# Kernel optimization log

Hardware: AMD Instinct MI355X
Metric: run time of the kernel (lower is better)

The kernel has to match this reference:

```python
import jax, jax.numpy as jnp
import numpy as np

MIN_ROUGHNESS = 0.08
MAX_ROUGHNESS = 0.5
N_MIPS = 6  # 512 -> 16 cubemap mip chain


def _safe_normalize(x, eps=1e-20):
    return x * jax.lax.rsqrt(jnp.clip(jnp.sum(x * x, -1, keepdims=True), eps, None))


def _dot(a, b):
    return jnp.sum(a * b, -1, keepdims=True)


def _cube_face_uv(d):
    # nvdiffrast cube addressing (matches util.cube_to_dir face layout)
    x, y, z = d[..., 0], d[..., 1], d[..., 2]
    ax, ay, az = jnp.abs(x), jnp.abs(y), jnp.abs(z)
    is_x = (ax >= ay) & (ax >= az)
    is_y = (~is_x) & (ay >= az)
    face = jnp.where(is_x, jnp.where(x >= 0, 0, 1),
           jnp.where(is_y, jnp.where(y >= 0, 2, 3), jnp.where(z >= 0, 4, 5)))
    ma = jnp.maximum(jnp.where(is_x, ax, jnp.where(is_y, ay, az)), 1e-20)
    u = jnp.where(face == 0, -z, jnp.where(face == 1, z, jnp.where(face == 5, -x, x))) / ma
    v = jnp.where(face == 2, z, jnp.where(face == 3, -z, -y)) / ma
    return face, u, v


def _bilinear_cube(tex, face, u, v):
    # tex: [6,R,R,C]; face/u/v: [...]; edge-clamped bilinear within the face
    R = tex.shape[1]
    tu = (u * 0.5 + 0.5) * R - 0.5
    tv = (v * 0.5 + 0.5) * R - 0.5
    x0 = jnp.floor(tu); y0 = jnp.floor(tv)
    fx = (tu - x0)[..., None]; fy = (tv - y0)[..., None]
    x0i = jnp.clip(x0, 0, R - 1).astype(jnp.int32)
    x1i = jnp.clip(x0 + 1, 0, R - 1).astype(jnp.int32)
    y0i = jnp.clip(y0, 0, R - 1).astype(jnp.int32)
    y1i = jnp.clip(y0 + 1, 0, R - 1).astype(jnp.int32)
    c00 = tex[face, y0i, x0i]; c01 = tex[face, y0i, x1i]
    c10 = tex[face, y1i, x0i]; c11 = tex[face, y1i, x1i]
    return (c00 * (1 - fx) + c01 * fx) * (1 - fy) + (c10 * (1 - fx) + c11 * fx) * fy


def _sample_cubemap(tex, dirs):
    f, u, v = _cube_face_uv(dirs)
    return _bilinear_cube(tex, f, u, v)


def _sample_2d_clamp(tex, uv):
    # tex: [H,W,C]; uv in [0,1]^2, clamp boundary bilinear (FG LUT lookup)
    H, W = tex.shape[0], tex.shape[1]
    tu = uv[..., 0] * W - 0.5
    tv = uv[..., 1] * H - 0.5
    x0 = jnp.floor(tu); y0 = jnp.floor(tv)
    fx = (tu - x0)[..., None]; fy = (tv - y0)[..., None]
    x0i = jnp.clip(x0, 0, W - 1).astype(jnp.int32)
    x1i = jnp.clip(x0 + 1, 0, W - 1).astype(jnp.int32)
    y0i = jnp.clip(y0, 0, H - 1).astype(jnp.int32)
    y1i = jnp.clip(y0 + 1, 0, H - 1).astype(jnp.int32)
    c00 = tex[y0i, x0i]; c01 = tex[y0i, x1i]
    c10 = tex[y1i, x0i]; c11 = tex[y1i, x1i]
    return (c00 * (1 - fx) + c01 * fx) * (1 - fy) + (c10 * (1 - fx) + c11 * fx) * fy


def _get_mip(r, n_levels):
    lo = (jnp.clip(r, MIN_ROUGHNESS, MAX_ROUGHNESS) - MIN_ROUGHNESS) / (MAX_ROUGHNESS - MIN_ROUGHNESS) * (n_levels - 2)
    hi = (jnp.clip(r, MAX_ROUGHNESS, 1.0) - MAX_ROUGHNESS) / (1.0 - MAX_ROUGHNESS) + (n_levels - 2)
    return jnp.where(r < MAX_ROUGHNESS, lo, hi)


def _linear2srgb(x):
    xs = jnp.where(x > 0.0031308, x, 1.0)  # avoid pow(0) grad issues
    return jnp.where(x > 0.0031308, 1.055 * jnp.power(xs, 1.0 / 2.4) - 0.055, 12.92 * x)


def _avg_pool_cube(c):
    F, R, _, C = c.shape
    return c.reshape(F, R // 2, 2, R // 2, 2, C).mean(axis=(2, 4))


def setup_inputs() -> dict:
    key = jax.random.key(0)
    ks = jax.random.split(key, 10)
    B, H, W = 1, 1024, 1024
    gb_pos = jax.random.normal(ks[0], (B, H, W, 3), jnp.float32)
    gb_normal = _safe_normalize(jax.random.normal(ks[1], (B, H, W, 3), jnp.float32))
    basecolor = jax.random.uniform(ks[2], (B, H, W, 3), jnp.float32)
    metallic = jax.random.uniform(ks[3], (B, H, W, 1), jnp.float32)
    roughness = jax.random.uniform(ks[4], (B, H, W, 1), jnp.float32)
    view_pos = jax.random.normal(ks[5], (1, 1, 1, 3), jnp.float32) * 3.0
    diffuse = jax.random.uniform(ks[6], (6, 16, 16, 3), jnp.float32)
    fg_lut = jax.random.uniform(ks[7], (256, 256, 2), jnp.float32)
    specs = {}
    s = jax.random.uniform(ks[8], (6, 512, 512, 3), jnp.float32)
    for l in range(N_MIPS):
        specs['spec%d' % l] = s
        if l < N_MIPS - 1:
            s = _avg_pool_cube(s)
    return dict(gb_pos=gb_pos, gb_normal=gb_normal, basecolor=basecolor,
                metallic=metallic, roughness=roughness, view_pos=view_pos,
                diffuse=diffuse, fg_lut=fg_lut, **specs)


def reference(gb_pos, gb_normal, basecolor, metallic, roughness, view_pos,
              diffuse, fg_lut, spec0, spec1, spec2, spec3, spec4, spec5):
    specs = [spec0, spec1, spec2, spec3, spec4, spec5]
    L = len(specs)
    metallic = metallic[..., :1]
    wo = _safe_normalize(view_pos - gb_pos)
    diffuse_albedo = (1.0 - metallic) * basecolor
    specular_albedo = 0.04 * (1.0 - metallic) + metallic * basecolor
    reflvec = _safe_normalize(2.0 * _dot(wo, gb_normal) * gb_normal - wo)
    # diffuse IBL: cubemap gather along normal
    ambient = _sample_cubemap(diffuse, gb_normal)
    diffuse_linear = ambient * diffuse_albedo
    # FG LUT gather
    NdotV = jnp.clip(_dot(wo, gb_normal), 1e-4, None)
    fg = _sample_2d_clamp(fg_lut, jnp.concatenate([NdotV, roughness], -1))
    # trilinear (linear-mipmap-linear) specular cubemap gather
    mip = jnp.clip(_get_mip(roughness[..., 0], L), 0.0, L - 1.0)
    face, u, v = _cube_face_uv(reflvec)
    spec = jnp.zeros(gb_pos.shape[:-1] + (spec0.shape[-1],), gb_pos.dtype)
    for l in range(L):
        w = jnp.clip(1.0 - jnp.abs(mip - l), 0.0, 1.0)[..., None]
        spec = spec + w * _bilinear_cube(specs[l], face, u, v)
    reflectance = specular_albedo * fg[..., 0:1] + fg[..., 1:2]
    rgb = spec * reflectance + diffuse_linear
    return _linear2srgb(jnp.clip(rgb, 0.0, 1.0))
```

## Files before the change

kernel.cpp:

```cpp
#include <hip/hip_runtime.h>

struct V3 { float x, y, z; };

__device__ __forceinline__ V3 v3add(V3 a, V3 b){ return {a.x+b.x, a.y+b.y, a.z+b.z}; }
__device__ __forceinline__ V3 v3sub(V3 a, V3 b){ return {a.x-b.x, a.y-b.y, a.z-b.z}; }
__device__ __forceinline__ V3 v3scale(V3 a, float s){ return {a.x*s, a.y*s, a.z*s}; }
__device__ __forceinline__ V3 v3mul(V3 a, V3 b){ return {a.x*b.x, a.y*b.y, a.z*b.z}; }
__device__ __forceinline__ float dot3(V3 a, V3 b){ return fmaf(a.x,b.x, fmaf(a.y,b.y, a.z*b.z)); }
__device__ __forceinline__ V3 nrm3(V3 a){
    float s = rsqrtf(fmaxf(dot3(a,a), 1e-20f));
    return v3scale(a, s);
}

__device__ __forceinline__ void cube_face_uv(V3 d, int& face, float& u, float& v){
    float ax = fabsf(d.x), ay = fabsf(d.y), az = fabsf(d.z);
    bool is_x = (ax >= ay) && (ax >= az);
    bool is_y = (!is_x) && (ay >= az);
    face = is_x ? (d.x >= 0.f ? 0 : 1)
                : (is_y ? (d.y >= 0.f ? 2 : 3)
                        : (d.z >= 0.f ? 4 : 5));
    float ma = fmaxf(is_x ? ax : (is_y ? ay : az), 1e-20f);
    float un = (face == 0) ? -d.z : (face == 1) ? d.z : (face == 5) ? -d.x : d.x;
    float vn = (face == 2) ?  d.z : (face == 3) ? -d.z : -d.y;
    float inv = 1.0f / ma;
    u = un * inv;
    v = vn * inv;
}

__device__ __forceinline__ V3 bilinear_cube3(const float* __restrict__ tex, int R,
                                             int face, float u, float v){
    float Rf = (float)R;
    float tu = fmaf(fmaf(u, 0.5f, 0.5f), Rf, -0.5f);
    float tv = fmaf(fmaf(v, 0.5f, 0.5f), Rf, -0.5f);
    float x0 = floorf(tu), y0 = floorf(tv);
    float fx = tu - x0,    fy = tv - y0;
    int x0i = min(max((int)x0,     0), R-1);
    int x1i = min(max((int)x0 + 1, 0), R-1);
    int y0i = min(max((int)y0,     0), R-1);
    int y1i = min(max((int)y0 + 1, 0), R-1);
    const float* base = tex + (size_t)face * R * R * 3;
    const float* r0 = base + (size_t)y0i * R * 3;
    const float* r1 = base + (size_t)y1i * R * 3;
    const float* p00 = r0 + 3*x0i;
    const float* p01 = r0 + 3*x1i;
    const float* p10 = r1 + 3*x0i;
    const float* p11 = r1 + 3*x1i;
    float a0 = p00[0], a1 = p00[1], a2 = p00[2];
    float b0 = p01[0], b1 = p01[1], b2 = p01[2];
    float c0 = p10[0], c1 = p10[1], c2 = p10[2];
    float d0 = p11[0], d1 = p11[1], d2 = p11[2];
    float w00 = (1.f-fx)*(1.f-fy), w01 = fx*(1.f-fy);
    float w10 = (1.f-fx)*fy,       w11 = fx*fy;
    V3 out;
    out.x = a0*w00 + b0*w01 + c0*w10 + d0*w11;
    out.y = a1*w00 + b1*w01 + c1*w10 + d1*w11;
    out.z = a2*w00 + b2*w01 + c2*w10 + d2*w11;
    return out;
}

__device__ __forceinline__ void sample_fg(const float* __restrict__ lut,
                                          float u, float v, float& fa, float& fb){
    const int W = 256, H = 256;
    float tu = fmaf(u, (float)W, -0.5f);
    float tv = fmaf(v, (float)H, -0.5f);
    float x0 = floorf(tu), y0 = floorf(tv);
    float fx = tu - x0,    fy = tv - y0;
    int x0i = min(max((int)x0,     0), W-1);
    int x1i = min(max((int)x0 + 1, 0), W-1);
    int y0i = min(max((int)y0,     0), H-1);
    int y1i = min(max((int)y0 + 1, 0), H-1);
    const float* r0 = lut + (size_t)y0i * W * 2;
    const float* r1 = lut + (size_t)y1i * W * 2;
    float a0 = r0[2*x0i], a1 = r0[2*x0i+1];
    float b0 = r0[2*x1i], b1 = r0[2*x1i+1];
    float c0 = r1[2*x0i], c1 = r1[2*x0i+1];
    float d0 = r1[2*x1i], d1 = r1[2*x1i+1];
    float w00 = (1.f-fx)*(1.f-fy), w01 = fx*(1.f-fy);
    float w10 = (1.f-fx)*fy,       w11 = fx*fy;
    fa = a0*w00 + b0*w01 + c0*w10 + d0*w11;
    fb = a1*w00 + b1*w01 + c1*w10 + d1*w11;
}

__device__ __forceinline__ float lin2srgb(float x){
    float xs = (x > 0.0031308f) ? x : 1.0f;
    float p  = __builtin_amdgcn_exp2f(__builtin_amdgcn_logf(xs) * (1.0f/2.4f));
    return (x > 0.0031308f) ? fmaf(1.055f, p, -0.055f) : 12.92f * x;
}

__device__ __forceinline__ float clamp01(float x){ return fminf(fmaxf(x, 0.f), 1.f); }

__global__ __launch_bounds__(256)
void envlight_kernel(const float* __restrict__ gb_pos,
                     const float* __restrict__ gb_normal,
                     const float* __restrict__ basecolor,
                     const float* __restrict__ metallic,
                     const float* __restrict__ roughness,
                     const float* __restrict__ view_pos,
                     const float* __restrict__ diffuse,
                     const float* __restrict__ fg_lut,
                     const float* __restrict__ s0,
                     const float* __restrict__ s1,
                     const float* __restrict__ s2,
                     const float* __restrict__ s3,
                     const float* __restrict__ s4,
                     const float* __restrict__ s5,
                     float* __restrict__ out,
                     int n)
{
    int i = blockIdx.x * blockDim.x + threadIdx.x;
    if (i >= n) return;

    V3 pos = { gb_pos[3*i],    gb_pos[3*i+1],    gb_pos[3*i+2] };
    V3 nrm = { gb_normal[3*i], gb_normal[3*i+1], gb_normal[3*i+2] };
    V3 bc  = { basecolor[3*i], basecolor[3*i+1], basecolor[3*i+2] };
    float m = metallic[i];
    float r = roughness[i];
    V3 vp  = { view_pos[0], view_pos[1], view_pos[2] };

    V3 wo = nrm3(v3sub(vp, pos));
    float ndv_raw = dot3(wo, nrm);
    V3 refl = nrm3(v3sub(v3scale(nrm, 2.0f*ndv_raw), wo));

    float one_m = 1.0f - m;
    V3 diff_alb = v3scale(bc, one_m);
    V3 spec_alb = { fmaf(m, bc.x, 0.04f*one_m),
                    fmaf(m, bc.y, 0.04f*one_m),
                    fmaf(m, bc.z, 0.04f*one_m) };

    int dface; float du, dv;
    cube_face_uv(nrm, dface, du, dv);
    V3 ambient = bilinear_cube3(diffuse, 16, dface, du, dv);

    float NdotV = fmaxf(ndv_raw, 0.0001f);
    float fa, fb;
    sample_fg(fg_lut, NdotV, r, fa, fb);

    const float MIN_R = 0.08f, MAX_R = 0.5f;
    float lo = (fminf(fmaxf(r, MIN_R), MAX_R) - MIN_R) / (MAX_R - MIN_R) * 4.0f;
    float hi = (fminf(fmaxf(r, MAX_R), 1.0f) - MAX_R) / (1.0f - MAX_R) + 4.0f;
    float mip = (r < MAX_R) ? lo : hi;
    mip = fminf(fmaxf(mip, 0.0f), 5.0f);

    int l0 = min((int)mip, 5);
    float f = mip - (float)l0;
    int l1 = min(l0 + 1, 5);

    const float* tA = s0;
    tA = (l0 == 1) ? s1 : tA; tA = (l0 == 2) ? s2 : tA;
    tA = (l0 == 3) ? s3 : tA; tA = (l0 == 4) ? s4 : tA; tA = (l0 == 5) ? s5 : tA;
    const float* tB = s0;
    tB = (l1 == 1) ? s1 : tB; tB = (l1 == 2) ? s2 : tB;
    tB = (l1 == 3) ? s3 : tB; tB = (l1 == 4) ? s4 : tB; tB = (l1 == 5) ? s5 : tB;
    int RA = 512 >> l0;
    int RB = 512 >> l1;

    int sface; float su, sv;
    cube_face_uv(refl, sface, su, sv);
    V3 specA = bilinear_cube3(tA, RA, sface, su, sv);
    V3 specB = bilinear_cube3(tB, RB, sface, su, sv);
    V3 spec = { specA.x + (specB.x - specA.x) * f,
                specA.y + (specB.y - specA.y) * f,
                specA.z + (specB.z - specA.z) * f };

    V3 reflc = { fmaf(spec_alb.x, fa, fb),
                 fmaf(spec_alb.y, fa, fb),
                 fmaf(spec_alb.z, fa, fb) };
    V3 rgb = v3add(v3mul(spec, reflc), v3mul(ambient, diff_alb));

    out[3*i+0] = lin2srgb(clamp01(rgb.x));
    out[3*i+1] = lin2srgb(clamp01(rgb.y));
    out[3*i+2] = lin2srgb(clamp01(rgb.z));
}

extern "C" void kernel_launch(void* const* d_in, const int* in_sizes, int n_in,
                              void* d_out, int out_size, void* d_ws, size_t ws_size,
                              hipStream_t stream) {
    const float* gb_pos    = (const float*)d_in[0];
    const float* gb_normal = (const float*)d_in[1];
    const float* basecolor = (const float*)d_in[2];
    const float* metallic  = (const float*)d_in[3];
    const float* roughness = (const float*)d_in[4];
    const float* view_pos  = (const float*)d_in[5];
    const float* diffuse   = (const float*)d_in[6];
    const float* fg_lut    = (const float*)d_in[7];
    const float* s0        = (const float*)d_in[8];
    const float* s1        = (const float*)d_in[9];
    const float* s2        = (const float*)d_in[10];
    const float* s3        = (const float*)d_in[11];
    const float* s4        = (const float*)d_in[12];
    const float* s5        = (const float*)d_in[13];
    float* out = (float*)d_out;

    int n = in_sizes[0] / 3;
    int block = 256;
    int grid = (n + block - 1) / block;
    envlight_kernel<<<grid, block, 0, stream>>>(gb_pos, gb_normal, basecolor,
        metallic, roughness, view_pos, diffuse, fg_lut,
        s0, s1, s2, s3, s4, s5, out, n);
}
```

Measured before the change: 176.0 us.

## Repack cubemap mips into padded float4 workspace for vectorized texel gathers

Adds a pre-pass kernel that copies all six specular mip levels and the diffuse cubemap into one contiguous float4 workspace. The shading kernel then fetches each texel with a single 16-byte load instead of three scalar loads, and the FG LUT is read as float2. The repack runs every call, about 2.1M texels with 25MB read and 33MB written, so its cost may rival the gather savings. The original path is kept as a fallback when the workspace is too small.

```diff
diff --git a/kernel.cpp b/kernel.cpp
--- a/kernel.cpp
+++ b/kernel.cpp
@@ -11,6 +11,16 @@
     float s = rsqrtf(fmaxf(dot3(a,a), 1e-20f));
     return v3scale(a, s);
 }
+
+#define OFF0 0
+#define OFF1 1572864
+#define OFF2 1966080
+#define OFF3 2064384
+#define OFF4 2088960
+#define OFF5 2095104
+#define DIFF_OFF 2096640
+#define TOTAL_TEXELS 2098176
+#define WS_BYTES_NEEDED (TOTAL_TEXELS * 16)
 
 __device__ __forceinline__ void cube_face_uv(V3 d, int& face, float& u, float& v){
     float ax = fabsf(d.x), ay = fabsf(d.y), az = fabsf(d.z);
@@ -27,34 +37,61 @@
     v = vn * inv;
 }
 
-__device__ __forceinline__ V3 bilinear_cube3(const float* __restrict__ tex, int R,
-                                             int face, float u, float v){
+struct BilinCoord { int x0i, x1i, y0i, y1i; float fx, fy; };
+
+__device__ __forceinline__ BilinCoord bilin_coord(float u, float v, int R){
     float Rf = (float)R;
     float tu = fmaf(fmaf(u, 0.5f, 0.5f), Rf, -0.5f);
     float tv = fmaf(fmaf(v, 0.5f, 0.5f), Rf, -0.5f);
     float x0 = floorf(tu), y0 = floorf(tv);
-    float fx = tu - x0,    fy = tv - y0;
-    int x0i = min(max((int)x0,     0), R-1);
-    int x1i = min(max((int)x0 + 1, 0), R-1);
-    int y0i = min(max((int)y0,     0), R-1);
-    int y1i = min(max((int)y0 + 1, 0), R-1);
+    BilinCoord c;
+    c.fx = tu - x0; c.fy = tv - y0;
+    c.x0i = min(max((int)x0,     0), R-1);
+    c.x1i = min(max((int)x0 + 1, 0), R-1);
+    c.y0i = min(max((int)y0,     0), R-1);
+    c.y1i = min(max((int)y0 + 1, 0), R-1);
+    return c;
+}
+
+__device__ __forceinline__ V3 bilinear_cube4(const float4* __restrict__ tex, int R,
+                                             int face, float u, float v){
+    BilinCoord c = bilin_coord(u, v, R);
+    const float4* base = tex + (size_t)face * R * R;
+    const float4* r0 = base + (size_t)c.y0i * R;
+    const float4* r1 = base + (size_t)c.y1i * R;
+    float4 a = r0[c.x0i];
+    float4 b = r0[c.x1i];
+    float4 d = r1[c.x0i];
+    float4 e = r1[c.x1i];
+    float w00 = (1.f-c.fx)*(1.f-c.fy), w01 = c.fx*(1.f-c.fy);
+    float w10 = (1.f-c.fx)*c.fy,       w11 = c.fx*c.fy;
+    V3 out;
+    out.x = a.x*w00 + b.x*w01 + d.x*w10 + e.x*w11;
+    out.y = a.y*w00 + b.y*w01 + d.y*w10 + e.y*w11;
+    out.z = a.z*w00 + b.z*w01 + d.z*w10 + e.z*w11;
+    return out;
+}
+
+__device__ __forceinline__ V3 bilinear_cube3(const float* __restrict__ tex, int R,
+                                             int face, float u, float v){
+    BilinCoord c = bilin_coord(u, v, R);
     const float* base = tex + (size_t)face * R * R * 3;
-    const float* r0 = base + (size_t)y0i * R * 3;
-    const float* r1 = base + (size_t)y1i * R * 3;
-    const float* p00 = r0 + 3*x0i;
-    const float* p01 = r0 + 3*x1i;
-    const float* p10 = r1 + 3*x0i;
-    const float* p11 = r1 + 3*x1i;
+    const float* r0 = base + (size_t)c.y0i * R * 3;
+    const float* r1 = base + (size_t)c.y1i * R * 3;
+    const float* p00 = r0 + 3*c.x0i;
+    const float* p01 = r0 + 3*c.x1i;
+    const float* p10 = r1 + 3*c.x0i;
+    const float* p11 = r1 + 3*c.x1i;
     float a0 = p00[0], a1 = p00[1], a2 = p00[2];
     float b0 = p01[0], b1 = p01[1], b2 = p01[2];
-    float c0 = p10[0], c1 = p10[1], c2 = p10[2];
-    float d0 = p11[0], d1 = p11[1], d2 = p11[2];
-    float w00 = (1.f-fx)*(1.f-fy), w01 = fx*(1.f-fy);
-    float w10 = (1.f-fx)*fy,       w11 = fx*fy;
+    float d0 = p10[0], d1 = p10[1], d2 = p10[2];
+    float e0 = p11[0], e1 = p11[1], e2 = p11[2];
+    float w00 = (1.f-c.fx)*(1.f-c.fy), w01 = c.fx*(1.f-c.fy);
+    float w10 = (1.f-c.fx)*c.fy,       w11 = c.fx*c.fy;
     V3 out;
-    out.x = a0*w00 + b0*w01 + c0*w10 + d0*w11;
-    out.y = a1*w00 + b1*w01 + c1*w10 + d1*w11;
-    out.z = a2*w00 + b2*w01 + c2*w10 + d2*w11;
+    out.x = a0*w00 + b0*w01 + d0*w10 + e0*w11;
+    out.y = a1*w00 + b1*w01 + d1*w10 + e1*w11;
+    out.z = a2*w00 + b2*w01 + d2*w10 + e2*w11;
     return out;
 }
 
@@ -69,16 +106,15 @@
     int x1i = min(max((int)x0 + 1, 0), W-1);
     int y0i = min(max((int)y0,     0), H-1);
     int y1i = min(max((int)y0 + 1, 0), H-1);
-    const float* r0 = lut + (size_t)y0i * W * 2;
-    const float* r1 = lut + (size_t)y1i * W * 2;
-    float a0 = r0[2*x0i], a1 = r0[2*x0i+1];
-    float b0 = r0[2*x1i], b1 = r0[2*x1i+1];
-    float c0 = r1[2*x0i], c1 = r1[2*x0i+1];
-    float d0 = r1[2*x1i], d1 = r1[2*x1i+1];
+    const float2* l2 = (const float2*)lut;
+    float2 a = l2[(size_t)y0i*W + x0i];
+    float2 b = l2[(size_t)y0i*W + x1i];
+    float2 d = l2[(size_t)y1i*W + x0i];
+    float2 e = l2[(size_t)y1i*W + x1i];
     float w00 = (1.f-fx)*(1.f-fy), w01 = fx*(1.f-fy);
     float w10 = (1.f-fx)*fy,       w11 = fx*fy;
-    fa = a0*w00 + b0*w01 + c0*w10 + d0*w11;
-    fb = a1*w00 + b1*w01 + c1*w10 + d1*w11;
+    fa = a.x*w00 + b.x*w01 + d.x*w10 + e.x*w11;
+    fb = a.y*w00 + b.y*w01 + d.y*w10 + e.y*w11;
 }
 
 __device__ __forceinline__ float lin2srgb(float x){
@@ -89,6 +125,114 @@
 
 __device__ __forceinline__ float clamp01(float x){ return fminf(fmaxf(x, 0.f), 1.f); }
 
+__global__ __launch_bounds__(256)
+void pack_kernel(const float* __restrict__ s0, const float* __restrict__ s1,
+                 const float* __restrict__ s2, const float* __restrict__ s3,
+                 const float* __restrict__ s4, const float* __restrict__ s5,
+                 const float* __restrict__ diffuse,
+                 float4* __restrict__ ws)
+{
+    int t = blockIdx.x * blockDim.x + threadIdx.x;
+    if (t >= TOTAL_TEXELS) return;
+    const float* src; int local;
+    if      (t >= DIFF_OFF) { src = diffuse; local = t - DIFF_OFF; }
+    else if (t >= OFF5)     { src = s5;      local = t - OFF5; }
+    else if (t >= OFF4)     { src = s4;      local = t - OFF4; }
+    else if (t >= OFF3)     { src = s3;      local = t - OFF3; }
+    else if (t >= OFF2)     { src = s2;      local = t - OFF2; }
+    else if (t >= OFF1)     { src = s1;      local = t - OFF1; }
+    else                    { src = s0;      local = t; }
+    float a = src[3*local], b = src[3*local+1], c = src[3*local+2];
+    ws[t] = make_float4(a, b, c, 0.f);
+}
+
+template <bool PACKED>
+__device__ __forceinline__ void shade_pixel(
+    int i,
+    const float* __restrict__ gb_pos, const float* __restrict__ gb_normal,
+    const float* __restrict__ basecolor, const float* __restrict__ metallic,
+    const float* __restrict__ roughness, const float* __restrict__ view_pos,
+    const float* __restrict__ diffuse, const float* __restrict__ fg_lut,
+    const float* __restrict__ s0, const float* __restrict__ s1,
+    const float* __restrict__ s2, const float* __restrict__ s3,
+    const float* __restrict__ s4, const float* __restrict__ s5,
+    const float4* __restrict__ ws,
+    float* __restrict__ out)
+{
+    V3 pos = { gb_pos[3*i],    gb_pos[3*i+1],    gb_pos[3*i+2] };
+    V3 nrm = { gb_normal[3*i], gb_normal[3*i+1], gb_normal[3*i+2] };
+    V3 bc  = { basecolor[3*i], basecolor[3*i+1], basecolor[3*i+2] };
+    float m = metallic[i];
+    float r = roughness[i];
+    V3 vp  = { view_pos[0], view_pos[1], view_pos[2] };
+
+    V3 wo = nrm3(v3sub(vp, pos));
+    float ndv_raw = dot3(wo, nrm);
+    V3 refl = nrm3(v3sub(v3scale(nrm, 2.0f*ndv_raw), wo));
+
+    float one_m = 1.0f - m;
+    V3 diff_alb = v3scale(bc, one_m);
+    V3 spec_alb = { fmaf(m, bc.x, 0.04f*one_m),
+                    fmaf(m, bc.y, 0.04f*one_m),
+                    fmaf(m, bc.z, 0.04f*one_m) };
+
+    const float MIN_R = 0.08f, MAX_R = 0.5f;
+    float lo = (fminf(fmaxf(r, MIN_R), MAX_R) - MIN_R) / (MAX_R - MIN_R) * 4.0f;
+    float hi = (fminf(fmaxf(r, MAX_R), 1.0f) - MAX_R) / (1.0f - MAX_R) + 4.0f;
+    float mip = (r < MAX_R) ? lo : hi;
+    mip = fminf(fmaxf(mip, 0.0f), 5.0f);
+    int l0 = min((int)mip, 5);
+    float f = mip - (float)l0;
+    int l1 = min(l0 + 1, 5);
+
+    int dface; float du, dv;
+    cube_face_uv(nrm, dface, du, dv);
+    int sface; float su, sv;
+    cube_face_uv(refl, sface, su, sv);
+    float NdotV = fmaxf(ndv_raw, 0.0001f);
+
+    V3 ambient, specA, specB;
+    if (PACKED) {
+        int offA = OFF0;
+        offA = (l0 == 1) ? OFF1 : offA; offA = (l0 == 2) ? OFF2 : offA;
+        offA = (l0 == 3) ? OFF3 : offA; offA = (l0 == 4) ? OFF4 : offA;
+        offA = (l0 == 5) ? OFF5 : offA;
+        int offB = OFF0;
+        offB = (l1 == 1) ? OFF1 : offB; offB = (l1 == 2) ? OFF2 : offB;
+        offB = (l1 == 3) ? OFF3 : offB; offB = (l1 == 4) ? OFF4 : offB;
+        offB = (l1 == 5) ? OFF5 : offB;
+        ambient = bilinear_cube4(ws + DIFF_OFF, 16, dface, du, dv);
+        specA   = bilinear_cube4(ws + offA, 512 >> l0, sface, su, sv);
+        specB   = bilinear_cube4(ws + offB, 512 >> l1, sface, su, sv);
+    } else {
+        const float* tA = s0;
+        tA = (l0 == 1) ? s1 : tA; tA = (l0 == 2) ? s2 : tA;
+        tA = (l0 == 3) ? s3 : tA; tA = (l0 == 4) ? s4 : tA; tA = (l0 == 5) ? s5 : tA;
+        const float* tB = s0;
+        tB = (l1 == 1) ? s1 : tB; tB = (l1 == 2) ? s2 : tB;
+        tB = (l1 == 3) ? s3 : tB; tB = (l1 == 4) ? s4 : tB; tB = (l1 == 5) ? s5 : tB;
+        ambient = bilinear_cube3(diffuse, 16, dface, du, dv);
+        specA   = bilinear_cube3(tA, 512 >> l0, sface, su, sv);
+        specB   = bilinear_cube3(tB, 512 >> l1, sface, su, sv);
+    }
+
+    float fa, fb;
+    sample_fg(fg_lut, NdotV, r, fa, fb);
+
+    V3 spec = { specA.x + (specB.x - specA.x) * f,
+                specA.y + (specB.y - specA.y) * f,
+                specA.z + (specB.z - specA.z) * f };
+    V3 reflc = { fmaf(spec_alb.x, fa, fb),
+                 fmaf(spec_alb.y, fa, fb),
+                 fmaf(spec_alb.z, fa, fb) };
+    V3 rgb = v3add(v3mul(spec, reflc), v3mul(ambient, diff_alb));
+
+    out[3*i+0] = lin2srgb(clamp01(rgb.x));
+    out[3*i+1] = lin2srgb(clamp01(rgb.y));
+    out[3*i+2] = lin2srgb(clamp01(rgb.z));
+}
+
+template <bool PACKED>
 __global__ __launch_bounds__(256)
 void envlight_kernel(const float* __restrict__ gb_pos,
                      const float* __restrict__ gb_normal,
@@ -104,72 +248,14 @@
                      const float* __restrict__ s3,
                      const float* __restrict__ s4,
                      const float* __restrict__ s5,
+                     const float4* __restrict__ ws,
                      float* __restrict__ out,
                      int n)
 {
     int i = blockIdx.x * blockDim.x + threadIdx.x;
     if (i >= n) return;
-
-    V3 pos = { gb_pos[3*i],    gb_pos[3*i+1],    gb_pos[3*i+2] };
-    V3 nrm = { gb_normal[3*i], gb_normal[3*i+1], gb_normal[3*i+2] };
-    V3 bc  = { basecolor[3*i], basecolor[3*i+1], basecolor[3*i+2] };
-    float m = metallic[i];
-    float r = roughness[i];
-    V3 vp  = { view_pos[0], view_pos[1], view_pos[2] };
-
-    V3 wo = nrm3(v3sub(vp, pos));
-    float ndv_raw = dot3(wo, nrm);
-    V3 refl = nrm3(v3sub(v3scale(nrm, 2.0f*ndv_raw), wo));
-
-    float one_m = 1.0f - m;
-    V3 diff_alb = v3scale(bc, one_m);
-    V3 spec_alb = { fmaf(m, bc.x, 0.04f*one_m),
-                    fmaf(m, bc.y, 0.04f*one_m),
-                    fmaf(m, bc.z, 0.04f*one_m) };
-
-    int dface; float du, dv;
-    cube_face_uv(nrm, dface, du, dv);
-    V3 ambient = bilinear_cube3(diffuse, 16, dface, du, dv);
-
-    float NdotV = fmaxf(ndv_raw, 0.0001f);
-    float fa, fb;
-    sample_fg(fg_lut, NdotV, r, fa, fb);
-
-    const float MIN_R = 0.08f, MAX_R = 0.5f;
-    float lo = (fminf(fmaxf(r, MIN_R), MAX_R) - MIN_R) / (MAX_R - MIN_R) * 4.0f;
-    float hi = (fminf(fmaxf(r, MAX_R), 1.0f) - MAX_R) / (1.0f - MAX_R) + 4.0f;
-    float mip = (r < MAX_R) ? lo : hi;
-    mip = fminf(fmaxf(mip, 0.0f), 5.0f);
-
-    int l0 = min((int)mip, 5);
-    float f = mip - (float)l0;
-    int l1 = min(l0 + 1, 5);
-
-    const float* tA = s0;
-    tA = (l0 == 1) ? s1 : tA; tA = (l0 == 2) ? s2 : tA;
-    tA = (l0 == 3) ? s3 : tA; tA = (l0 == 4) ? s4 : tA; tA = (l0 == 5) ? s5 : tA;
-    const float* tB = s0;
-    tB = (l1 == 1) ? s1 : tB; tB = (l1 == 2) ? s2 : tB;
-    tB = (l1 == 3) ? s3 : tB; tB = (l1 == 4) ? s4 : tB; tB = (l1 == 5) ? s5 : tB;
-    int RA = 512 >> l0;
-    int RB = 512 >> l1;
-
-    int sface; float su, sv;
-    cube_face_uv(refl, sface, su, sv);
-    V3 specA = bilinear_cube3(tA, RA, sface, su, sv);
-    V3 specB = bilinear_cube3(tB, RB, sface, su, sv);
-    V3 spec = { specA.x + (specB.x - specA.x) * f,
-                specA.y + (specB.y - specA.y) * f,
-                specA.z + (specB.z - specA.z) * f };
-
-    V3 reflc = { fmaf(spec_alb.x, fa, fb),
-                 fmaf(spec_alb.y, fa, fb),
-                 fmaf(spec_alb.z, fa, fb) };
-    V3 rgb = v3add(v3mul(spec, reflc), v3mul(ambient, diff_alb));
-
-    out[3*i+0] = lin2srgb(clamp01(rgb.x));
-    out[3*i+1] = lin2srgb(clamp01(rgb.y));
-    out[3*i+2] = lin2srgb(clamp01(rgb.z));
+    shade_pixel<PACKED>(i, gb_pos, gb_normal, basecolor, metallic, roughness,
+                        view_pos, diffuse, fg_lut, s0, s1, s2, s3, s4, s5, ws, out);
 }
 
 extern "C" void kernel_launch(void* const* d_in, const int* in_sizes, int n_in,
@@ -194,7 +280,17 @@
     int n = in_sizes[0] / 3;
     int block = 256;
     int grid = (n + block - 1) / block;
-    envlight_kernel<<<grid, block, 0, stream>>>(gb_pos, gb_normal, basecolor,
-        metallic, roughness, view_pos, diffuse, fg_lut,
-        s0, s1, s2, s3, s4, s5, out, n);
-}
+
+    if (ws_size >= (size_t)WS_BYTES_NEEDED) {
+        float4* ws = (float4*)d_ws;
+        int pgrid = (TOTAL_TEXELS + block - 1) / block;
+        pack_kernel<<<pgrid, block, 0, stream>>>(s0, s1, s2, s3, s4, s5, diffuse, ws);
+        envlight_kernel<true><<<grid, block, 0, stream>>>(gb_pos, gb_normal, basecolor,
+            metallic, roughness, view_pos, diffuse, fg_lut,
+            s0, s1, s2, s3, s4, s5, ws, out, n);
+    } else {
+        envlight_kernel<false><<<grid, block, 0, stream>>>(gb_pos, gb_normal, basecolor,
+            metallic, roughness, view_pos, diffuse, fg_lut,
+            s0, s1, s2, s3, s4, s5, (const float4*)nullptr, out, n);
+    }
+}
```

Measured after the change: 184.2 us. 1.05x slower.
